# Optimization experiments

Measured on AMD Instinct MI355X. Metric: run time of the kernel, lower is better.

The kernel has to match this reference:

```python
import jax, jax.numpy as jnp
import numpy as np

OFFSETS = (1, 2, 4, 8, 16, 64, 96, 192, 384, 512, 768, 1024)
J = 12
J_LARGE = 8  # offsets with index >= 4 use phase rotation


def _shift(x, d):
    """Return x shifted so out[..., n, :] = x[..., n-d, :]; zeros where n < d.
    Shift is along axis 2 (the sequence axis of [B,H,N,...])."""
    pad = [(0, 0)] * x.ndim
    pad[2] = (d, 0)
    return jnp.pad(x, pad)[:, :, : x.shape[2]]


def setup_inputs() -> dict:
    key = jax.random.key(0)
    ks = jax.random.split(key, 9)
    B, H, N, HD = 2, 16, 4096, 64
    f = jnp.float32
    q = jax.random.normal(ks[0], (B, H, N, HD), f)
    k = jax.random.normal(ks[1], (B, H, N, HD), f)
    v = jax.random.normal(ks[2], (B, H, N, HD), f)
    pb = jax.random.normal(ks[3], (J, H), f) * 0.1          # per-offset per-head score bias
    se = jax.random.normal(ks[4], (J, HD), f) * 0.1         # per-offset score embedding
    phase_base = jax.random.normal(ks[5], (J_LARGE, H, 2), f) * 0.1
    phase_gain = jax.random.normal(ks[6], (J_LARGE, H, 2), f) * 0.1
    y_pre = jax.random.normal(ks[7], (B, H, N, 2), f)       # query-side phase features
    z_pre = jax.random.normal(ks[8], (B, H, N, 2), f)       # key-side phase features
    return dict(q=q, k=k, v=v, pb=pb, se=se, phase_base=phase_base,
                phase_gain=phase_gain, y_pre=y_pre, z_pre=z_pre)


def reference(q, k, v, pb, se, phase_base, phase_gain, y_pre, z_pre):
    B, H, N, HD = q.shape
    sc = 1.0 / float(np.sqrt(HD))
    n_idx = jnp.arange(N)

    # --- scores over the J fixed causal offsets: s_i[n] = (q_n . (k_{n-d} + se_i)) * sc + pb[i,h]
    scores = []
    for i, d in enumerate(OFFSETS):
        ks_ = _shift(k, d)  # key at n - d
        s = (jnp.einsum('bhnd,bhnd->bhn', q, ks_)
             + jnp.einsum('bhnd,d->bhn', q, se[i])) * sc
        s = s + pb[i][None, :, None]
        valid = (n_idx >= d)[None, None, :]
        scores.append(jnp.where(valid, s, -jnp.inf))
    scores = jnp.stack(scores, axis=-1)  # [B,H,N,J]

    lse = jax.nn.logsumexp(scores, axis=-1)            # [B,H,N]
    safe_lse = jnp.where(jnp.isfinite(lse), lse, 0.0)  # rows with no valid offset -> alpha = 0
    alpha = jnp.exp(scores - safe_lse[..., None])      # [B,H,N,J]; -inf scores give exactly 0

    # --- weighted sum of (phase-rotated) values
    out = jnp.zeros_like(q)
    for i, d in enumerate(OFFSETS):
        vs = _shift(v, d)  # value at n - d: [B,H,N,HD]
        if i >= 4:
            pi = i - 4
            zs = _shift(z_pre, d)  # key-side phase features at n - d: [B,H,N,2]
            # theta_p = base[pi,h,p] + gain[pi,h,p] * y_pre[n,p] * z_pre[n-d,p]
            theta = (phase_base[pi][None, :, None, :]
                     + phase_gain[pi][None, :, None, :] * y_pre * zs)  # [B,H,N,2]
            c, s_ = jnp.cos(theta), jnp.sin(theta)
            v0, v1, v2, v3 = vs[..., 0], vs[..., 1], vs[..., 2], vs[..., 3]
            rot = jnp.stack([c[..., 0] * v0 - s_[..., 0] * v1,
                             s_[..., 0] * v0 + c[..., 0] * v1,
                             c[..., 1] * v2 - s_[..., 1] * v3,
                             s_[..., 1] * v2 + c[..., 1] * v3], axis=-1)
            vs = jnp.concatenate([rot, vs[..., 4:]], axis=-1)
        out = out + alpha[..., i:i + 1] * vs
    return out
```

## Files before the change

kernel.cpp:

```cpp
#include <hip/hip_runtime.h>


namespace {

constexpr int J   = 12;
constexpr int B_  = 2;
constexpr int H_  = 16;
constexpr int N_  = 4096;
constexpr int HD_ = 64;
constexpr int OFFS[J] = {1, 2, 4, 8, 16, 64, 96, 192, 384, 512, 768, 1024};

__global__ __launch_bounds__(256) void dsqg_kernel(
    const float* __restrict__ q, const float* __restrict__ k,
    const float* __restrict__ v, const float* __restrict__ pb,
    const float* __restrict__ se, const float* __restrict__ phase_base,
    const float* __restrict__ phase_gain, const float* __restrict__ y_pre,
    const float* __restrict__ z_pre, float* __restrict__ out)
{
    const int raw = blockIdx.x;
    const int per = gridDim.x >> 3;
    const int wid = (raw & 7) * per + (raw >> 3);

    const int bh    = wid >> 8;
    const int chunk = wid & 255;
    const int h     = bh & (H_ - 1);

    const int lane = threadIdx.x & 63;
    const int wave = threadIdx.x >> 6;
    const int grp  = lane & 15;
    const int n    = chunk * 16 + wave * 4 + (lane >> 4);

    const size_t base4 = (size_t)bh * N_ * (HD_ / 4);
    const float4* q4 = (const float4*)q + base4;
    const float4* k4 = (const float4*)k + base4;
    const float4* v4 = (const float4*)v + base4;
    float4*       o4 = (float4*)out + base4;

    const float4 qr = q4[(size_t)n * 16 + grp];

    int m[J];
    bool ok[J];
#pragma unroll
    for (int i = 0; i < J; ++i) {
        ok[i] = (n >= OFFS[i]);
        m[i]  = ok[i] ? (n - OFFS[i]) : 0;
    }

    float2 zr[8];
    float2 yp = make_float2(0.f, 0.f);
    if (grp == 0) {
        yp = ((const float2*)y_pre)[(size_t)bh * N_ + n];
#pragma unroll
        for (int pi = 0; pi < 8; ++pi)
            zr[pi] = ((const float2*)z_pre)[(size_t)bh * N_ + m[pi + 4]];
    }

    float4 kr[J];
#pragma unroll
    for (int i = 0; i < J; ++i) kr[i] = k4[(size_t)m[i] * 16 + grp];

    float p[J];
#pragma unroll
    for (int i = 0; i < J; ++i) {
        const float4 seg = ((const float4*)se)[i * 16 + grp];
        float t = qr.x * seg.x + qr.y * seg.y + qr.z * seg.z + qr.w * seg.w;
        t = fmaf(qr.x, kr[i].x, t);
        t = fmaf(qr.y, kr[i].y, t);
        t = fmaf(qr.z, kr[i].z, t);
        p[i] = fmaf(qr.w, kr[i].w, t);
    }

    float4 vr[J];
#pragma unroll
    for (int i = 0; i < J; ++i) vr[i] = v4[(size_t)m[i] * 16 + grp];

#pragma unroll
    for (int stage = 1; stage <= 8; stage <<= 1) {
#pragma unroll
        for (int i = 0; i < J; ++i) p[i] += __shfl_xor(p[i], stage);
    }

    const float sc = 0.125f;
    float e[J];
    float sum = 0.f;
#pragma unroll
    for (int i = 0; i < J; ++i) {
        const float si = fmaf(p[i], sc, pb[i * H_ + h]);
        e[i] = ok[i] ? __expf(si) : 0.f;
        sum += e[i];
    }

    if (grp == 0) {
#pragma unroll
        for (int pi = 0; pi < 8; ++pi) {
            const int i = pi + 4;
            const float b0 = phase_base[(pi * H_ + h) * 2 + 0];
            const float b1 = phase_base[(pi * H_ + h) * 2 + 1];
            const float g0 = phase_gain[(pi * H_ + h) * 2 + 0];
            const float g1 = phase_gain[(pi * H_ + h) * 2 + 1];
            const float th0 = fmaf(g0, yp.x * zr[pi].x, b0);
            const float th1 = fmaf(g1, yp.y * zr[pi].y, b1);
            const float c0 = __cosf(th0), s0 = __sinf(th0);
            const float c1 = __cosf(th1), s1 = __sinf(th1);
            const float v0 = vr[i].x, v1 = vr[i].y, v2 = vr[i].z, v3 = vr[i].w;
            vr[i].x = c0 * v0 - s0 * v1;
            vr[i].y = s0 * v0 + c0 * v1;
            vr[i].z = c1 * v2 - s1 * v3;
            vr[i].w = s1 * v2 + c1 * v3;
        }
    }

    float4 acc = make_float4(0.f, 0.f, 0.f, 0.f);
#pragma unroll
    for (int i = 0; i < J; ++i) {
        acc.x = fmaf(e[i], vr[i].x, acc.x);
        acc.y = fmaf(e[i], vr[i].y, acc.y);
        acc.z = fmaf(e[i], vr[i].z, acc.z);
        acc.w = fmaf(e[i], vr[i].w, acc.w);
    }

    float4 res;
    if (n >= 1) {
        const float inv = 1.0f / sum;
        res = make_float4(acc.x * inv, acc.y * inv, acc.z * inv, acc.w * inv);
    } else {
        res = make_float4(0.f, 0.f, 0.f, 0.f);
    }
    o4[(size_t)n * 16 + grp] = res;
}

}

extern "C" void kernel_launch(void* const* d_in, const int* in_sizes, int n_in,
                              void* d_out, int out_size, void* d_ws, size_t ws_size,
                              hipStream_t stream) {
    const float* q          = (const float*)d_in[0];
    const float* k          = (const float*)d_in[1];
    const float* v          = (const float*)d_in[2];
    const float* pb         = (const float*)d_in[3];
    const float* se         = (const float*)d_in[4];
    const float* phase_base = (const float*)d_in[5];
    const float* phase_gain = (const float*)d_in[6];
    const float* y_pre      = (const float*)d_in[7];
    const float* z_pre      = (const float*)d_in[8];
    float* out              = (float*)d_out;

    const int positions = B_ * H_ * N_;
    const int blocks    = positions / 16;
    dsqg_kernel<<<blocks, 256, 0, stream>>>(q, k, v, pb, se, phase_base,
                                            phase_gain, y_pre, z_pre, out);
}
```

Measured before the change: 190.1 us.

## Spread phase rotation across lanes, use DPP row reductions, and specialize unmasked chunks

Before, lane 0 of each 16-lane group did all eight phase rotations and z_pre loads serially. Now each lane in the group handles one offset's head-of-vector slice: it rotates it where needed, weights it, and the results are combined with DPP row reductions. The shuffle-based dot-product reductions become DPP adds, and the kernel is templated so chunks beyond the largest offset skip all masking logic. Launch bounds are set to 4 blocks per CU, which may restrict registers, and the extra per-lane head loads and cross-lane reductions add some ALU work.

```diff
diff --git a/kernel.cpp b/kernel.cpp
--- a/kernel.cpp
+++ b/kernel.cpp
@@ -7,10 +7,143 @@
 constexpr int B_  = 2;
 constexpr int H_  = 16;
 constexpr int N_  = 4096;
-constexpr int HD_ = 64;
 constexpr int OFFS[J] = {1, 2, 4, 8, 16, 64, 96, 192, 384, 512, 768, 1024};
 
-__global__ __launch_bounds__(256) void dsqg_kernel(
+template <int CTRL>
+__device__ __forceinline__ float dpp_add(float x) {
+    int t = __builtin_amdgcn_update_dpp(0, __float_as_int(x), CTRL, 0xf, 0xf, true);
+    return x + __int_as_float(t);
+}
+
+__device__ __forceinline__ float row16_reduce(float x) {
+    x = dpp_add<0xB1>(x);
+    x = dpp_add<0x4E>(x);
+    x = dpp_add<0x141>(x);
+    x = dpp_add<0x140>(x);
+    return x;
+}
+
+template <bool MASKED>
+__device__ __forceinline__ void body(
+    int n, int grp, int h, size_t bhN,
+    const float4* __restrict__ q4, const float4* __restrict__ k4,
+    const float4* __restrict__ v4, float4* __restrict__ o4,
+    const float* __restrict__ pb, const float4* __restrict__ se4,
+    const float2* __restrict__ pbase2, const float2* __restrict__ pgain2,
+    const float2* __restrict__ y2, const float2* __restrict__ z2)
+{
+    const float4 qr = q4[(size_t)n * 16 + grp];
+
+    int m[J];
+#pragma unroll
+    for (int i = 0; i < J; ++i) {
+        if (MASKED) m[i] = (n >= OFFS[i]) ? (n - OFFS[i]) : 0;
+        else        m[i] = n - OFFS[i];
+    }
+
+    const int g = grp;
+    int dg = 16;
+    dg = (g == 1) ? 64   : dg;
+    dg = (g == 2) ? 96   : dg;
+    dg = (g == 3) ? 192  : dg;
+    dg = (g == 4) ? 384  : dg;
+    dg = (g == 5) ? 512  : dg;
+    dg = (g == 6) ? 768  : dg;
+    dg = (g == 7) ? 1024 : dg;
+    dg = (g == 8) ? 1    : dg;
+    dg = (g == 9) ? 2    : dg;
+    dg = (g == 10) ? 4   : dg;
+    dg = (g == 11) ? 8   : dg;
+    int mg = n - dg;
+    mg = (mg < 0) ? 0 : mg;
+
+    const float2 yp    = y2[bhN + n];
+    const float4 vhead = v4[(size_t)mg * 16];
+    const float2 zg    = z2[bhN + mg];
+    const int    pi8   = g & 7;
+    const float2 pbse  = pbase2[pi8 * H_ + h];
+    const float2 pgn   = pgain2[pi8 * H_ + h];
+
+    float4 kr[J];
+#pragma unroll
+    for (int i = 0; i < J; ++i) kr[i] = k4[(size_t)m[i] * 16 + grp];
+    float4 vr[J];
+#pragma unroll
+    for (int i = 0; i < J; ++i) vr[i] = v4[(size_t)m[i] * 16 + grp];
+
+    float p[J];
+#pragma unroll
+    for (int i = 0; i < J; ++i) {
+        const float4 seg = se4[i * 16 + grp];
+        float t;
+        t = qr.x * (kr[i].x + seg.x);
+        t = fmaf(qr.y, kr[i].y + seg.y, t);
+        t = fmaf(qr.z, kr[i].z + seg.z, t);
+        t = fmaf(qr.w, kr[i].w + seg.w, t);
+        p[i] = row16_reduce(t);
+    }
+
+    float e[J];
+    float sum = 0.f;
+#pragma unroll
+    for (int i = 0; i < J; ++i) {
+        const float si = fmaf(p[i], 0.125f, pb[i * H_ + h]);
+        const bool ok = MASKED ? (n >= OFFS[i]) : true;
+        e[i] = ok ? __expf(si) : 0.f;
+        sum += e[i];
+    }
+
+    float esel = e[4];
+    esel = (g == 1) ? e[5]  : esel;
+    esel = (g == 2) ? e[6]  : esel;
+    esel = (g == 3) ? e[7]  : esel;
+    esel = (g == 4) ? e[8]  : esel;
+    esel = (g == 5) ? e[9]  : esel;
+    esel = (g == 6) ? e[10] : esel;
+    esel = (g == 7) ? e[11] : esel;
+    esel = (g == 8) ? e[0]  : esel;
+    esel = (g == 9) ? e[1]  : esel;
+    esel = (g == 10) ? e[2] : esel;
+    esel = (g == 11) ? e[3] : esel;
+
+    const float th0 = fmaf(pgn.x, yp.x * zg.x, pbse.x);
+    const float th1 = fmaf(pgn.y, yp.y * zg.y, pbse.y);
+    const float c0 = __cosf(th0), s0 = __sinf(th0);
+    const float c1 = __cosf(th1), s1 = __sinf(th1);
+
+    const bool isrot = (g < 8);
+    float cx = isrot ? (c0 * vhead.x - s0 * vhead.y) : vhead.x;
+    float cy = isrot ? (s0 * vhead.x + c0 * vhead.y) : vhead.y;
+    float cz = isrot ? (c1 * vhead.z - s1 * vhead.w) : vhead.z;
+    float cw = isrot ? (s1 * vhead.z + c1 * vhead.w) : vhead.w;
+    const float wgt = (g < 12) ? esel : 0.f;
+    cx *= wgt; cy *= wgt; cz *= wgt; cw *= wgt;
+    cx = row16_reduce(cx);
+    cy = row16_reduce(cy);
+    cz = row16_reduce(cz);
+    cw = row16_reduce(cw);
+
+    float4 acc = make_float4(0.f, 0.f, 0.f, 0.f);
+#pragma unroll
+    for (int i = 0; i < J; ++i) {
+        acc.x = fmaf(e[i], vr[i].x, acc.x);
+        acc.y = fmaf(e[i], vr[i].y, acc.y);
+        acc.z = fmaf(e[i], vr[i].z, acc.z);
+        acc.w = fmaf(e[i], vr[i].w, acc.w);
+    }
+    if (g == 0) { acc.x = cx; acc.y = cy; acc.z = cz; acc.w = cw; }
+
+    float4 res;
+    if (!MASKED || n >= 1) {
+        const float inv = 1.0f / sum;
+        res = make_float4(acc.x * inv, acc.y * inv, acc.z * inv, acc.w * inv);
+    } else {
+        res = make_float4(0.f, 0.f, 0.f, 0.f);
+    }
+    o4[(size_t)n * 16 + grp] = res;
+}
+
+__global__ __launch_bounds__(256, 4) void dsqg_kernel(
     const float* __restrict__ q, const float* __restrict__ k,
     const float* __restrict__ v, const float* __restrict__ pb,
     const float* __restrict__ se, const float* __restrict__ phase_base,
@@ -30,103 +163,22 @@
     const int grp  = lane & 15;
     const int n    = chunk * 16 + wave * 4 + (lane >> 4);
 
-    const size_t base4 = (size_t)bh * N_ * (HD_ / 4);
+    const size_t base4 = (size_t)bh * N_ * 16;
     const float4* q4 = (const float4*)q + base4;
     const float4* k4 = (const float4*)k + base4;
     const float4* v4 = (const float4*)v + base4;
     float4*       o4 = (float4*)out + base4;
-
-    const float4 qr = q4[(size_t)n * 16 + grp];
-
-    int m[J];
-    bool ok[J];
-#pragma unroll
-    for (int i = 0; i < J; ++i) {
-        ok[i] = (n >= OFFS[i]);
-        m[i]  = ok[i] ? (n - OFFS[i]) : 0;
-    }
-
-    float2 zr[8];
-    float2 yp = make_float2(0.f, 0.f);
-    if (grp == 0) {
-        yp = ((const float2*)y_pre)[(size_t)bh * N_ + n];
-#pragma unroll
-        for (int pi = 0; pi < 8; ++pi)
-            zr[pi] = ((const float2*)z_pre)[(size_t)bh * N_ + m[pi + 4]];
-    }
-
-    float4 kr[J];
-#pragma unroll
-    for (int i = 0; i < J; ++i) kr[i] = k4[(size_t)m[i] * 16 + grp];
-
-    float p[J];
-#pragma unroll
-    for (int i = 0; i < J; ++i) {
-        const float4 seg = ((const float4*)se)[i * 16 + grp];
-        float t = qr.x * seg.x + qr.y * seg.y + qr.z * seg.z + qr.w * seg.w;
-        t = fmaf(qr.x, kr[i].x, t);
-        t = fmaf(qr.y, kr[i].y, t);
-        t = fmaf(qr.z, kr[i].z, t);
-        p[i] = fmaf(qr.w, kr[i].w, t);
-    }
-
-    float4 vr[J];
-#pragma unroll
-    for (int i = 0; i < J; ++i) vr[i] = v4[(size_t)m[i] * 16 + grp];
-
-#pragma unroll
-    for (int stage = 1; stage <= 8; stage <<= 1) {
-#pragma unroll
-        for (int i = 0; i < J; ++i) p[i] += __shfl_xor(p[i], stage);
-    }
-
-    const float sc = 0.125f;
-    float e[J];
-    float sum = 0.f;
-#pragma unroll
-    for (int i = 0; i < J; ++i) {
-        const float si = fmaf(p[i], sc, pb[i * H_ + h]);
-        e[i] = ok[i] ? __expf(si) : 0.f;
-        sum += e[i];
-    }
-
-    if (grp == 0) {
-#pragma unroll
-        for (int pi = 0; pi < 8; ++pi) {
-            const int i = pi + 4;
-            const float b0 = phase_base[(pi * H_ + h) * 2 + 0];
-            const float b1 = phase_base[(pi * H_ + h) * 2 + 1];
-            const float g0 = phase_gain[(pi * H_ + h) * 2 + 0];
-            const float g1 = phase_gain[(pi * H_ + h) * 2 + 1];
-            const float th0 = fmaf(g0, yp.x * zr[pi].x, b0);
-            const float th1 = fmaf(g1, yp.y * zr[pi].y, b1);
-            const float c0 = __cosf(th0), s0 = __sinf(th0);
-            const float c1 = __cosf(th1), s1 = __sinf(th1);
-            const float v0 = vr[i].x, v1 = vr[i].y, v2 = vr[i].z, v3 = vr[i].w;
-            vr[i].x = c0 * v0 - s0 * v1;
-            vr[i].y = s0 * v0 + c0 * v1;
-            vr[i].z = c1 * v2 - s1 * v3;
-            vr[i].w = s1 * v2 + c1 * v3;
-        }
-    }
-
-    float4 acc = make_float4(0.f, 0.f, 0.f, 0.f);
-#pragma unroll
-    for (int i = 0; i < J; ++i) {
-        acc.x = fmaf(e[i], vr[i].x, acc.x);
-        acc.y = fmaf(e[i], vr[i].y, acc.y);
-        acc.z = fmaf(e[i], vr[i].z, acc.z);
-        acc.w = fmaf(e[i], vr[i].w, acc.w);
-    }
-
-    float4 res;
-    if (n >= 1) {
-        const float inv = 1.0f / sum;
-        res = make_float4(acc.x * inv, acc.y * inv, acc.z * inv, acc.w * inv);
+    const size_t bhN = (size_t)bh * N_;
+
+    if (chunk >= 64) {
+        body<false>(n, grp, h, bhN, q4, k4, v4, o4, pb, (const float4*)se,
+                    (const float2*)phase_base, (const float2*)phase_gain,
+                    (const float2*)y_pre, (const float2*)z_pre);
     } else {
-        res = make_float4(0.f, 0.f, 0.f, 0.f);
-    }
-    o4[(size_t)n * 16 + grp] = res;
+        body<true>(n, grp, h, bhN, q4, k4, v4, o4, pb, (const float4*)se,
+                   (const float2*)phase_base, (const float2*)phase_gain,
+                   (const float2*)y_pre, (const float2*)z_pre);
+    }
 }
 
 }
```

Result: no change. 193.3 us (+1.7%).
